# Optimization experiments

Measured on AMD Instinct MI355X. Metric: run time of the kernel, lower is better.

Reference implementation:

```python
import jax, jax.numpy as jnp
import numpy as np

B, H, L, D = 4, 16, 2048, 64


def setup_inputs() -> dict:
    key = jax.random.key(0)
    k1, k2, k3 = jax.random.split(key, 3)
    return {
        "query": jax.random.normal(k1, (B, H, L, D), dtype=jnp.float32),
        "key": jax.random.normal(k2, (B, H, L, D), dtype=jnp.float32),
        "value": jax.random.normal(k3, (B, H, D, L), dtype=jnp.float32),
    }


def reference(query, key, value):
    # dot_product_score = Q @ K^T / sqrt(D)   -> [B,H,L,L]
    d = query.shape[-1]
    scores = jnp.einsum("bhqd,bhkd->bhqk", query, key) / jnp.sqrt(jnp.asarray(d, query.dtype))
    attn = jax.nn.softmax(scores, axis=-1)
    # NOTE: original module returns matmul(value, attention_score) = V @ A
    # (value contracted over its last dim L with attn's query dim L) -> [B,H,D,L]
    return jnp.matmul(value, attn)
```

## Files before the change

### kernel.cpp

```cpp
#include <hip/hip_runtime.h>
#include <hip/hip_bf16.h>

#define L_SEQ 2048
#define D_HEAD 64
#define NHEADS 64
#define QSCALE (0.125f * 1.44269504088896340736f)

typedef __attribute__((ext_vector_type(8))) __bf16 bf16x8;
typedef __attribute__((ext_vector_type(16))) float f32x16;

__device__ __forceinline__ int swz(int row, int col) {
    int off = (row << 7) | (col << 1);
    return off ^ ((row & 7) << 4);
}
__device__ __forceinline__ bf16x8 read_frag(const char* lds, int row, int col) {
    return *reinterpret_cast<const bf16x8*>(lds + swz(row, col));
}

template <int ROWS>
__device__ __forceinline__ void stage_load(float4* regs, const float* src,
                                           int srcStride, int t) {
    int r0 = t >> 4, c4 = (t & 15) << 2;
#pragma unroll
    for (int i = 0; i < ROWS / 16; ++i)
        regs[i] = *reinterpret_cast<const float4*>(src + (size_t)(r0 + i * 16) * srcStride + c4);
}
template <int ROWS>
__device__ __forceinline__ void stage_write(char* lds, const float4* regs, int t,
                                            float scale) {
    int r0 = t >> 4, c4 = (t & 15) << 2;
#pragma unroll
    for (int i = 0; i < ROWS / 16; ++i) {
        float4 v = regs[i];
        union { __bf16 h[4]; unsigned long long u; } pk;
        pk.h[0] = (__bf16)(v.x * scale);
        pk.h[1] = (__bf16)(v.y * scale);
        pk.h[2] = (__bf16)(v.z * scale);
        pk.h[3] = (__bf16)(v.w * scale);
        *reinterpret_cast<unsigned long long*>(lds + swz(r0 + i * 16, c4)) = pk.u;
    }
}

__device__ __forceinline__ unsigned cvt_pk_bf16(float lo, float hi) {
    unsigned r;
    asm("v_cvt_pk_bf16_f32 %0, %1, %2" : "=v"(r) : "v"(lo), "v"(hi));
    return r;
}

__global__ __launch_bounds__(256, 3) void attn_pass1(const float* __restrict__ Q,
                                                     const float* __restrict__ K,
                                                     float* __restrict__ invl) {
    __shared__ __align__(16) char lds[2][128 * 128];
    __shared__ float red[4][64];

    int bid = blockIdx.x;
    int sb = (bid & 7) * 256 + (bid >> 3);
    int bh = sb >> 5;
    int q0 = (sb & 31) << 6;
    const float* Qh = Q + (size_t)bh * L_SEQ * D_HEAD + (size_t)q0 * D_HEAD;
    const float* Kh = K + (size_t)bh * L_SEQ * D_HEAD;

    int t = threadIdx.x, lane = t & 63, w = t >> 6;
    int hl = lane >> 5, l31 = lane & 31;

    {
        float4 qreg[4];
        stage_load<64>(qreg, Qh, D_HEAD, t);
        stage_write<64>(lds[0], qreg, t, QSCALE);
    }
    __syncthreads();
    bf16x8 qfrag[2][4];
#pragma unroll
    for (int qb = 0; qb < 2; ++qb)
#pragma unroll
        for (int m = 0; m < 4; ++m)
            qfrag[qb][m] = read_frag(lds[0], qb * 32 + l31, m * 16 + hl * 8);
    __syncthreads();
    {
        float4 kreg[8];
        stage_load<128>(kreg, Kh, D_HEAD, t);
        stage_write<128>(lds[0], kreg, t, 1.0f);
    }
    __syncthreads();

    float lsum[2][16];
#pragma unroll
    for (int qb = 0; qb < 2; ++qb)
#pragma unroll
        for (int r = 0; r < 16; ++r) lsum[qb][r] = 0.f;

    for (int k0 = 0; k0 < L_SEQ; k0 += 128) {
        int c = (k0 >> 7) & 1;
        const char* kcur = lds[c];
        char* knext = lds[c ^ 1];

        int nk0 = (k0 + 128) & (L_SEQ - 1);
        float4 kreg[8];
        stage_load<128>(kreg, Kh + (size_t)nk0 * D_HEAD, D_HEAD, t);

        bf16x8 kfr[4];
#pragma unroll
        for (int m = 0; m < 4; ++m)
            kfr[m] = read_frag(kcur, w * 32 + l31, m * 16 + hl * 8);

        f32x16 s[2];
#pragma unroll
        for (int qb = 0; qb < 2; ++qb)
#pragma unroll
            for (int r = 0; r < 16; ++r) s[qb][r] = 0.f;

        __builtin_amdgcn_s_setprio(1);
#pragma unroll
        for (int m = 0; m < 4; ++m) {
            s[0] = __builtin_amdgcn_mfma_f32_32x32x16_bf16(qfrag[0][m], kfr[m], s[0], 0, 0, 0);
            s[1] = __builtin_amdgcn_mfma_f32_32x32x16_bf16(qfrag[1][m], kfr[m], s[1], 0, 0, 0);
        }
        __builtin_amdgcn_s_setprio(0);

#pragma unroll
        for (int qb = 0; qb < 2; ++qb)
#pragma unroll
            for (int r = 0; r < 16; ++r)
                lsum[qb][r] += __builtin_amdgcn_exp2f(s[qb][r]);

        stage_write<128>(knext, kreg, t, 1.0f);
        __syncthreads();
    }

#pragma unroll
    for (int qb = 0; qb < 2; ++qb)
#pragma unroll
        for (int r = 0; r < 16; ++r) {
            float v = lsum[qb][r];
            v += __shfl_xor(v, 1);
            v += __shfl_xor(v, 2);
            v += __shfl_xor(v, 4);
            v += __shfl_xor(v, 8);
            v += __shfl_xor(v, 16);
            lsum[qb][r] = v;
        }
    if (l31 == 0) {
#pragma unroll
        for (int qb = 0; qb < 2; ++qb)
#pragma unroll
            for (int r = 0; r < 16; ++r)
                red[w][qb * 32 + (r & 3) + 8 * (r >> 2) + 4 * hl] = lsum[qb][r];
    }
    __syncthreads();
    if (t < 64) {
        float ssum = red[0][t] + red[1][t] + red[2][t] + red[3][t];
        invl[(size_t)bh * L_SEQ + q0 + t] = 1.0f / ssum;
    }
}

__global__ __launch_bounds__(256, 2) void attn_pass2(const float* __restrict__ Q,
                                                     const float* __restrict__ K,
                                                     const float* __restrict__ V,
                                                     const float* __restrict__ invl,
                                                     float* __restrict__ out) {
    __shared__ __align__(16) char lds[32768];
    char* ldsQ0 = lds;
    char* ldsQ1 = lds + 8192;
    char* ldsV0 = lds + 16384;
    char* ldsV1 = lds + 24576;

    int bid = blockIdx.x;
    int sb = (bid & 7) * 64 + (bid >> 3);
    int bh = sb >> 3;
    int k0 = (sb & 7) << 8;
    const float* Qh = Q + (size_t)bh * L_SEQ * D_HEAD;
    const float* Kh = K + (size_t)bh * L_SEQ * D_HEAD + (size_t)k0 * D_HEAD;
    const float* Vh = V + (size_t)bh * D_HEAD * L_SEQ;
    const float* il = invl + (size_t)bh * L_SEQ;
    float* Oh = out + (size_t)bh * D_HEAD * L_SEQ;

    int t = threadIdx.x, lane = t & 63, w = t >> 6;
    int hl = lane >> 5, l31 = lane & 31;

    {
        float4 kreg[8];
        stage_load<128>(kreg, Kh, D_HEAD, t);
        stage_write<128>(lds, kreg, t, 1.0f);
        stage_load<128>(kreg, Kh + (size_t)128 * D_HEAD, D_HEAD, t);
        stage_write<128>(lds + 128 * 128, kreg, t, 1.0f);
    }
    __syncthreads();
    bf16x8 kfrag[2][4];
#pragma unroll
    for (int kb = 0; kb < 2; ++kb)
#pragma unroll
        for (int m = 0; m < 4; ++m)
            kfrag[kb][m] = read_frag(lds, w * 64 + kb * 32 + l31, m * 16 + hl * 8);
    __syncthreads();
    {
        float4 qreg[4], vreg[4];
        stage_load<64>(qreg, Qh, D_HEAD, t);
        stage_load<64>(vreg, Vh, L_SEQ, t);
        stage_write<64>(ldsQ0, qreg, t, QSCALE);
        stage_write<64>(ldsV0, vreg, t, 1.0f);
    }
    __syncthreads();

    f32x16 acc[2][2];
#pragma unroll
    for (int db = 0; db < 2; ++db)
#pragma unroll
        for (int kb = 0; kb < 2; ++kb)
#pragma unroll
            for (int r = 0; r < 16; ++r) acc[db][kb][r] = 0.f;

    for (int q0 = 0; q0 < L_SEQ; q0 += 64) {
        int c = (q0 >> 6) & 1;
        const char* qcur = c ? ldsQ1 : ldsQ0;
        const char* vcur = c ? ldsV1 : ldsV0;
        char* qnext = c ? ldsQ0 : ldsQ1;
        char* vnext = c ? ldsV0 : ldsV1;

        int nq0 = (q0 + 64) & (L_SEQ - 1);
        float4 qreg[4], vreg[4];
        stage_load<64>(qreg, Qh + (size_t)nq0 * D_HEAD, D_HEAD, t);
        stage_load<64>(vreg, Vh + nq0, L_SEQ, t);

#pragma unroll
        for (int qb = 0; qb < 2; ++qb) {
            union { float4 v4[4]; float f[16]; } ilu;
#pragma unroll
            for (int g = 0; g < 4; ++g)
                ilu.v4[g] = *reinterpret_cast<const float4*>(il + q0 + qb * 32 + 8 * g + 4 * hl);

            f32x16 s[2];
#pragma unroll
            for (int kb = 0; kb < 2; ++kb)
#pragma unroll
                for (int r = 0; r < 16; ++r) s[kb][r] = 0.f;

            __builtin_amdgcn_s_setprio(1);
#pragma unroll
            for (int m = 0; m < 4; ++m) {
                bf16x8 afr = read_frag(qcur, qb * 32 + l31, m * 16 + hl * 8);
                s[0] = __builtin_amdgcn_mfma_f32_32x32x16_bf16(afr, kfrag[0][m], s[0], 0, 0, 0);
                s[1] = __builtin_amdgcn_mfma_f32_32x32x16_bf16(afr, kfrag[1][m], s[1], 0, 0, 0);
            }
            __builtin_amdgcn_s_setprio(0);

            bf16x8 pfrag[2][2];
#pragma unroll
            for (int kb = 0; kb < 2; ++kb) {
                float p[16];
#pragma unroll
                for (int r = 0; r < 16; ++r)
                    p[r] = __builtin_amdgcn_exp2f(s[kb][r]) * ilu.f[r];
                unsigned wA[4], wB[4];
#pragma unroll
                for (int g = 0; g < 4; ++g) {
                    wA[g] = cvt_pk_bf16(p[4 * g + 0], p[4 * g + 1]);
                    wB[g] = cvt_pk_bf16(p[4 * g + 2], p[4 * g + 3]);
                }
#pragma unroll
                for (int mm = 0; mm < 2; ++mm) {
                    unsigned a0 = wA[2 * mm], b0 = wA[2 * mm + 1];
                    unsigned a1 = wB[2 * mm], b1 = wB[2 * mm + 1];
                    asm volatile("v_permlane32_swap_b32 %0, %1" : "+v"(a0), "+v"(b0));
                    asm volatile("v_permlane32_swap_b32 %0, %1" : "+v"(a1), "+v"(b1));
                    union { unsigned u[4]; bf16x8 v; } pk;
                    pk.u[0] = a0;
                    pk.u[1] = a1;
                    pk.u[2] = b0;
                    pk.u[3] = b1;
                    pfrag[kb][mm] = pk.v;
                }
            }

            __builtin_amdgcn_s_setprio(1);
#pragma unroll
            for (int mm = 0; mm < 2; ++mm)
#pragma unroll
                for (int db = 0; db < 2; ++db) {
                    bf16x8 vfr = read_frag(vcur, db * 32 + l31, qb * 32 + mm * 16 + hl * 8);
#pragma unroll
                    for (int kb = 0; kb < 2; ++kb)
                        acc[db][kb] = __builtin_amdgcn_mfma_f32_32x32x16_bf16(
                            vfr, pfrag[kb][mm], acc[db][kb], 0, 0, 0);
                }
            __builtin_amdgcn_s_setprio(0);
        }

        stage_write<64>(qnext, qreg, t, QSCALE);
        stage_write<64>(vnext, vreg, t, 1.0f);
        __syncthreads();
    }

#pragma unroll
    for (int db = 0; db < 2; ++db)
#pragma unroll
        for (int kb = 0; kb < 2; ++kb)
#pragma unroll
            for (int r = 0; r < 16; ++r) {
                int d = db * 32 + (r & 3) + 8 * (r >> 2) + 4 * hl;
                int k = k0 + w * 64 + kb * 32 + l31;
                Oh[(size_t)d * L_SEQ + k] = acc[db][kb][r];
            }
}

extern "C" void kernel_launch(void* const* d_in, const int* in_sizes, int n_in,
                              void* d_out, int out_size, void* d_ws, size_t ws_size,
                              hipStream_t stream) {
    const float* Q = (const float*)d_in[0];
    const float* K = (const float*)d_in[1];
    const float* V = (const float*)d_in[2];
    float* invl = (float*)d_ws;
    float* out = (float*)d_out;

    attn_pass1<<<dim3(NHEADS * (L_SEQ / 64)), dim3(256), 0, stream>>>(Q, K, invl);
    attn_pass2<<<dim3(NHEADS * (L_SEQ / 256)), dim3(256), 0, stream>>>(Q, K, V, invl, out);
}
```

Measured before the change: 160.8 us.

## Split pass2 key tile over 8 waves and fold 1/l into V staging

Pass2 now launches 512 threads per block, so each of 8 waves owns 32 keys instead of 64. This halves per-wave accumulators and the K fragments held in registers, aiming for higher occupancy. The softmax normalizer 1/l is multiplied into V while it is converted to bf16 in LDS, which removes the per-element multiply after exp2. Each Q/V tile read from LDS is now shared by twice as many waves, which may add LDS traffic and barrier cost. Rounding V*invl to bf16 slightly changes precision.

```diff
diff --git a/kernel.cpp b/kernel.cpp
--- a/kernel.cpp
+++ b/kernel.cpp
@@ -41,6 +41,16 @@
     }
 }
 
+__device__ __forceinline__ void pack_write(char* lds, int row, int c4, float4 v,
+                                           float4 sc) {
+    union { __bf16 h[4]; unsigned long long u; } pk;
+    pk.h[0] = (__bf16)(v.x * sc.x);
+    pk.h[1] = (__bf16)(v.y * sc.y);
+    pk.h[2] = (__bf16)(v.z * sc.z);
+    pk.h[3] = (__bf16)(v.w * sc.w);
+    *reinterpret_cast<unsigned long long*>(lds + swz(row, c4)) = pk.u;
+}
+
 __device__ __forceinline__ unsigned cvt_pk_bf16(float lo, float hi) {
     unsigned r;
     asm("v_cvt_pk_bf16_f32 %0, %1, %2" : "=v"(r) : "v"(lo), "v"(hi));
@@ -153,16 +163,12 @@
     }
 }
 
-__global__ __launch_bounds__(256, 2) void attn_pass2(const float* __restrict__ Q,
+__global__ __launch_bounds__(512, 4) void attn_pass2(const float* __restrict__ Q,
                                                      const float* __restrict__ K,
                                                      const float* __restrict__ V,
                                                      const float* __restrict__ invl,
                                                      float* __restrict__ out) {
     __shared__ __align__(16) char lds[32768];
-    char* ldsQ0 = lds;
-    char* ldsQ1 = lds + 8192;
-    char* ldsV0 = lds + 16384;
-    char* ldsV1 = lds + 24576;
 
     int bid = blockIdx.x;
     int sb = (bid & 7) * 64 + (bid >> 3);
@@ -176,130 +182,123 @@
 
     int t = threadIdx.x, lane = t & 63, w = t >> 6;
     int hl = lane >> 5, l31 = lane & 31;
+    int r0 = t >> 4;
+    int c4 = (t & 15) << 2;
+
+#pragma unroll
+    for (int i = 0; i < 8; ++i) {
+        float4 v = *reinterpret_cast<const float4*>(Kh + (size_t)(r0 + i * 32) * D_HEAD + c4);
+        pack_write(lds, r0 + i * 32, c4, v, make_float4(1.f, 1.f, 1.f, 1.f));
+    }
+    __syncthreads();
+    bf16x8 kfrag[4];
+#pragma unroll
+    for (int m = 0; m < 4; ++m)
+        kfrag[m] = read_frag(lds, w * 32 + l31, m * 16 + hl * 8);
+    __syncthreads();
 
     {
-        float4 kreg[8];
-        stage_load<128>(kreg, Kh, D_HEAD, t);
-        stage_write<128>(lds, kreg, t, 1.0f);
-        stage_load<128>(kreg, Kh + (size_t)128 * D_HEAD, D_HEAD, t);
-        stage_write<128>(lds + 128 * 128, kreg, t, 1.0f);
-    }
-    __syncthreads();
-    bf16x8 kfrag[2][4];
-#pragma unroll
-    for (int kb = 0; kb < 2; ++kb)
-#pragma unroll
-        for (int m = 0; m < 4; ++m)
-            kfrag[kb][m] = read_frag(lds, w * 64 + kb * 32 + l31, m * 16 + hl * 8);
-    __syncthreads();
-    {
-        float4 qreg[4], vreg[4];
-        stage_load<64>(qreg, Qh, D_HEAD, t);
-        stage_load<64>(vreg, Vh, L_SEQ, t);
-        stage_write<64>(ldsQ0, qreg, t, QSCALE);
-        stage_write<64>(ldsV0, vreg, t, 1.0f);
-    }
-    __syncthreads();
-
-    f32x16 acc[2][2];
+        float4 qa = *reinterpret_cast<const float4*>(Qh + (size_t)r0 * D_HEAD + c4);
+        float4 qb = *reinterpret_cast<const float4*>(Qh + (size_t)(r0 + 32) * D_HEAD + c4);
+        float4 va = *reinterpret_cast<const float4*>(Vh + (size_t)r0 * L_SEQ + c4);
+        float4 vb = *reinterpret_cast<const float4*>(Vh + (size_t)(r0 + 32) * L_SEQ + c4);
+        float4 iv = *reinterpret_cast<const float4*>(il + c4);
+        float4 qs = make_float4(QSCALE, QSCALE, QSCALE, QSCALE);
+        pack_write(lds, r0, c4, qa, qs);
+        pack_write(lds, r0 + 32, c4, qb, qs);
+        pack_write(lds + 16384, r0, c4, va, iv);
+        pack_write(lds + 16384, r0 + 32, c4, vb, iv);
+    }
+    __syncthreads();
+
+    f32x16 acc[2];
 #pragma unroll
     for (int db = 0; db < 2; ++db)
 #pragma unroll
-        for (int kb = 0; kb < 2; ++kb)
-#pragma unroll
-            for (int r = 0; r < 16; ++r) acc[db][kb][r] = 0.f;
+        for (int r = 0; r < 16; ++r) acc[db][r] = 0.f;
 
     for (int q0 = 0; q0 < L_SEQ; q0 += 64) {
         int c = (q0 >> 6) & 1;
-        const char* qcur = c ? ldsQ1 : ldsQ0;
-        const char* vcur = c ? ldsV1 : ldsV0;
-        char* qnext = c ? ldsQ0 : ldsQ1;
-        char* vnext = c ? ldsV0 : ldsV1;
+        const char* qcur = c ? lds + 8192 : lds;
+        const char* vcur = c ? lds + 24576 : lds + 16384;
+        char* qnext = c ? lds : lds + 8192;
+        char* vnext = c ? lds + 16384 : lds + 24576;
 
         int nq0 = (q0 + 64) & (L_SEQ - 1);
-        float4 qreg[4], vreg[4];
-        stage_load<64>(qreg, Qh + (size_t)nq0 * D_HEAD, D_HEAD, t);
-        stage_load<64>(vreg, Vh + nq0, L_SEQ, t);
-
-#pragma unroll
-        for (int qb = 0; qb < 2; ++qb) {
-            union { float4 v4[4]; float f[16]; } ilu;
-#pragma unroll
-            for (int g = 0; g < 4; ++g)
-                ilu.v4[g] = *reinterpret_cast<const float4*>(il + q0 + qb * 32 + 8 * g + 4 * hl);
-
-            f32x16 s[2];
-#pragma unroll
-            for (int kb = 0; kb < 2; ++kb)
-#pragma unroll
-                for (int r = 0; r < 16; ++r) s[kb][r] = 0.f;
+        float4 qra = *reinterpret_cast<const float4*>(Qh + (size_t)(nq0 + r0) * D_HEAD + c4);
+        float4 qrb = *reinterpret_cast<const float4*>(Qh + (size_t)(nq0 + r0 + 32) * D_HEAD + c4);
+        float4 vra = *reinterpret_cast<const float4*>(Vh + (size_t)r0 * L_SEQ + nq0 + c4);
+        float4 vrb = *reinterpret_cast<const float4*>(Vh + (size_t)(r0 + 32) * L_SEQ + nq0 + c4);
+        float4 ivn = *reinterpret_cast<const float4*>(il + nq0 + c4);
+
+#pragma unroll
+        for (int qq = 0; qq < 2; ++qq) {
+            f32x16 s;
+#pragma unroll
+            for (int r = 0; r < 16; ++r) s[r] = 0.f;
 
             __builtin_amdgcn_s_setprio(1);
 #pragma unroll
             for (int m = 0; m < 4; ++m) {
-                bf16x8 afr = read_frag(qcur, qb * 32 + l31, m * 16 + hl * 8);
-                s[0] = __builtin_amdgcn_mfma_f32_32x32x16_bf16(afr, kfrag[0][m], s[0], 0, 0, 0);
-                s[1] = __builtin_amdgcn_mfma_f32_32x32x16_bf16(afr, kfrag[1][m], s[1], 0, 0, 0);
+                bf16x8 afr = read_frag(qcur, qq * 32 + l31, m * 16 + hl * 8);
+                s = __builtin_amdgcn_mfma_f32_32x32x16_bf16(afr, kfrag[m], s, 0, 0, 0);
             }
             __builtin_amdgcn_s_setprio(0);
 
-            bf16x8 pfrag[2][2];
-#pragma unroll
-            for (int kb = 0; kb < 2; ++kb) {
-                float p[16];
-#pragma unroll
-                for (int r = 0; r < 16; ++r)
-                    p[r] = __builtin_amdgcn_exp2f(s[kb][r]) * ilu.f[r];
-                unsigned wA[4], wB[4];
-#pragma unroll
-                for (int g = 0; g < 4; ++g) {
-                    wA[g] = cvt_pk_bf16(p[4 * g + 0], p[4 * g + 1]);
-                    wB[g] = cvt_pk_bf16(p[4 * g + 2], p[4 * g + 3]);
-                }
-#pragma unroll
-                for (int mm = 0; mm < 2; ++mm) {
-                    unsigned a0 = wA[2 * mm], b0 = wA[2 * mm + 1];
-                    unsigned a1 = wB[2 * mm], b1 = wB[2 * mm + 1];
-                    asm volatile("v_permlane32_swap_b32 %0, %1" : "+v"(a0), "+v"(b0));
-                    asm volatile("v_permlane32_swap_b32 %0, %1" : "+v"(a1), "+v"(b1));
-                    union { unsigned u[4]; bf16x8 v; } pk;
-                    pk.u[0] = a0;
-                    pk.u[1] = a1;
-                    pk.u[2] = b0;
-                    pk.u[3] = b1;
-                    pfrag[kb][mm] = pk.v;
-                }
+            float p[16];
+#pragma unroll
+            for (int r = 0; r < 16; ++r) p[r] = __builtin_amdgcn_exp2f(s[r]);
+            unsigned wA[4], wB[4];
+#pragma unroll
+            for (int g = 0; g < 4; ++g) {
+                wA[g] = cvt_pk_bf16(p[4 * g + 0], p[4 * g + 1]);
+                wB[g] = cvt_pk_bf16(p[4 * g + 2], p[4 * g + 3]);
             }
+            bf16x8 pfrag[2];
+#pragma unroll
+            for (int mm = 0; mm < 2; ++mm) {
+                unsigned a0 = wA[2 * mm], b0 = wA[2 * mm + 1];
+                unsigned a1 = wB[2 * mm], b1 = wB[2 * mm + 1];
+                asm volatile("v_permlane32_swap_b32 %0, %1" : "+v"(a0), "+v"(b0));
+                asm volatile("v_permlane32_swap_b32 %0, %1" : "+v"(a1), "+v"(b1));
+                union { unsigned u[4]; bf16x8 v; } pk;
+                pk.u[0] = a0;
+                pk.u[1] = a1;
+                pk.u[2] = b0;
+                pk.u[3] = b1;
+                pfrag[mm] = pk.v;
+            }
 
             __builtin_amdgcn_s_setprio(1);
 #pragma unroll
             for (int mm = 0; mm < 2; ++mm)
 #pragma unroll
                 for (int db = 0; db < 2; ++db) {
-                    bf16x8 vfr = read_frag(vcur, db * 32 + l31, qb * 32 + mm * 16 + hl * 8);
-#pragma unroll
-                    for (int kb = 0; kb < 2; ++kb)
-                        acc[db][kb] = __builtin_amdgcn_mfma_f32_32x32x16_bf16(
-                            vfr, pfrag[kb][mm], acc[db][kb], 0, 0, 0);
+                    bf16x8 vfr = read_frag(vcur, db * 32 + l31, qq * 32 + mm * 16 + hl * 8);
+                    acc[db] = __builtin_amdgcn_mfma_f32_32x32x16_bf16(
+                        vfr, pfrag[mm], acc[db], 0, 0, 0);
                 }
             __builtin_amdgcn_s_setprio(0);
         }
 
-        stage_write<64>(qnext, qreg, t, QSCALE);
-        stage_write<64>(vnext, vreg, t, 1.0f);
+        {
+            float4 qs = make_float4(QSCALE, QSCALE, QSCALE, QSCALE);
+            pack_write(qnext, r0, c4, qra, qs);
+            pack_write(qnext, r0 + 32, c4, qrb, qs);
+            pack_write(vnext, r0, c4, vra, ivn);
+            pack_write(vnext, r0 + 32, c4, vrb, ivn);
+        }
         __syncthreads();
     }
 
 #pragma unroll
     for (int db = 0; db < 2; ++db)
 #pragma unroll
-        for (int kb = 0; kb < 2; ++kb)
-#pragma unroll
-            for (int r = 0; r < 16; ++r) {
-                int d = db * 32 + (r & 3) + 8 * (r >> 2) + 4 * hl;
-                int k = k0 + w * 64 + kb * 32 + l31;
-                Oh[(size_t)d * L_SEQ + k] = acc[db][kb][r];
-            }
+        for (int r = 0; r < 16; ++r) {
+            int d = db * 32 + (r & 3) + 8 * (r >> 2) + 4 * hl;
+            int k = k0 + w * 32 + l31;
+            Oh[(size_t)d * L_SEQ + k] = acc[db][r];
+        }
 }
 
 extern "C" void kernel_launch(void* const* d_in, const int* in_sizes, int n_in,
@@ -312,5 +311,5 @@
     float* out = (float*)d_out;
 
     attn_pass1<<<dim3(NHEADS * (L_SEQ / 64)), dim3(256), 0, stream>>>(Q, K, invl);
-    attn_pass2<<<dim3(NHEADS * (L_SEQ / 256)), dim3(256), 0, stream>>>(Q, K, V, invl, out);
-}
+    attn_pass2<<<dim3(NHEADS * (L_SEQ / 256)), dim3(512), 0, stream>>>(Q, K, V, invl, out);
+}
```

New measurement: 158.5 us. Within noise of the previous version (-1.4%).

## Split pass2 over 128-key tiles with query-split waves and fold 1/l into V

Applied to the files above, without the earlier changes.

Pass2 now gives each block 128 keys instead of 256, which doubles the grid. Each pair of waves shares a key slice while splitting the 64-query chunk in two, and the halves' partial outputs are reduced through LDS at the end. The softmax normalizer 1/l is now folded into V when it is converted to bf16 in LDS, so it is no longer multiplied into every probability in the inner loop. Occupancy is raised to 3 blocks per CU. In exchange, Q/V staging traffic per output doubles and the kernel adds an LDS reduction epilogue.

```diff
diff --git a/kernel.cpp b/kernel.cpp
--- a/kernel.cpp
+++ b/kernel.cpp
@@ -41,6 +41,16 @@
     }
 }
 
+__device__ __forceinline__ void pack_write(char* lds, int row, int c4, float4 v,
+                                           float4 sc) {
+    union { __bf16 h[4]; unsigned long long u; } pk;
+    pk.h[0] = (__bf16)(v.x * sc.x);
+    pk.h[1] = (__bf16)(v.y * sc.y);
+    pk.h[2] = (__bf16)(v.z * sc.z);
+    pk.h[3] = (__bf16)(v.w * sc.w);
+    *reinterpret_cast<unsigned long long*>(lds + swz(row, c4)) = pk.u;
+}
+
 __device__ __forceinline__ unsigned cvt_pk_bf16(float lo, float hi) {
     unsigned r;
     asm("v_cvt_pk_bf16_f32 %0, %1, %2" : "=v"(r) : "v"(lo), "v"(hi));
@@ -91,8 +101,8 @@
 
     for (int k0 = 0; k0 < L_SEQ; k0 += 128) {
         int c = (k0 >> 7) & 1;
-        const char* kcur = lds[c];
-        char* knext = lds[c ^ 1];
+        const char* kcur = c ? lds[1] : lds[0];
+        char* knext = c ? lds[0] : lds[1];
 
         int nk0 = (k0 + 128) & (L_SEQ - 1);
         float4 kreg[8];
@@ -153,21 +163,17 @@
     }
 }
 
-__global__ __launch_bounds__(256, 2) void attn_pass2(const float* __restrict__ Q,
+__global__ __launch_bounds__(256, 3) void attn_pass2(const float* __restrict__ Q,
                                                      const float* __restrict__ K,
                                                      const float* __restrict__ V,
                                                      const float* __restrict__ invl,
                                                      float* __restrict__ out) {
-    __shared__ __align__(16) char lds[32768];
-    char* ldsQ0 = lds;
-    char* ldsQ1 = lds + 8192;
-    char* ldsV0 = lds + 16384;
-    char* ldsV1 = lds + 24576;
+    __shared__ __align__(16) char lds[49152];
 
     int bid = blockIdx.x;
-    int sb = (bid & 7) * 64 + (bid >> 3);
-    int bh = sb >> 3;
-    int k0 = (sb & 7) << 8;
+    int sb = (bid & 7) * 128 + (bid >> 3);
+    int bh = sb >> 4;
+    int k0 = (sb & 15) << 7;
     const float* Qh = Q + (size_t)bh * L_SEQ * D_HEAD;
     const float* Kh = K + (size_t)bh * L_SEQ * D_HEAD + (size_t)k0 * D_HEAD;
     const float* Vh = V + (size_t)bh * D_HEAD * L_SEQ;
@@ -175,14 +181,15 @@
     float* Oh = out + (size_t)bh * D_HEAD * L_SEQ;
 
     int t = threadIdx.x, lane = t & 63, w = t >> 6;
+    int wq = w >> 1, wk = w & 1;
     int hl = lane >> 5, l31 = lane & 31;
+    int r0 = t >> 4;
+    int c4 = (t & 15) << 2;
 
     {
         float4 kreg[8];
         stage_load<128>(kreg, Kh, D_HEAD, t);
         stage_write<128>(lds, kreg, t, 1.0f);
-        stage_load<128>(kreg, Kh + (size_t)128 * D_HEAD, D_HEAD, t);
-        stage_write<128>(lds + 128 * 128, kreg, t, 1.0f);
     }
     __syncthreads();
     bf16x8 kfrag[2][4];
@@ -190,14 +197,19 @@
     for (int kb = 0; kb < 2; ++kb)
 #pragma unroll
         for (int m = 0; m < 4; ++m)
-            kfrag[kb][m] = read_frag(lds, w * 64 + kb * 32 + l31, m * 16 + hl * 8);
-    __syncthreads();
+            kfrag[kb][m] = read_frag(lds, wk * 64 + kb * 32 + l31, m * 16 + hl * 8);
+
     {
         float4 qreg[4], vreg[4];
         stage_load<64>(qreg, Qh, D_HEAD, t);
         stage_load<64>(vreg, Vh, L_SEQ, t);
-        stage_write<64>(ldsQ0, qreg, t, QSCALE);
-        stage_write<64>(ldsV0, vreg, t, 1.0f);
+        float4 iv = *reinterpret_cast<const float4*>(il + c4);
+        float4 qs = make_float4(QSCALE, QSCALE, QSCALE, QSCALE);
+#pragma unroll
+        for (int i = 0; i < 4; ++i) {
+            pack_write(lds + 16384, r0 + i * 16, c4, qreg[i], qs);
+            pack_write(lds + 24576, r0 + i * 16, c4, vreg[i], iv);
+        }
     }
     __syncthreads();
 
@@ -211,95 +223,109 @@
 
     for (int q0 = 0; q0 < L_SEQ; q0 += 64) {
         int c = (q0 >> 6) & 1;
-        const char* qcur = c ? ldsQ1 : ldsQ0;
-        const char* vcur = c ? ldsV1 : ldsV0;
-        char* qnext = c ? ldsQ0 : ldsQ1;
-        char* vnext = c ? ldsV0 : ldsV1;
+        const char* qcur = lds + (c ? 32768 : 16384);
+        const char* vcur = lds + (c ? 40960 : 24576);
+        char* qnext = lds + (c ? 16384 : 32768);
+        char* vnext = lds + (c ? 24576 : 40960);
 
         int nq0 = (q0 + 64) & (L_SEQ - 1);
         float4 qreg[4], vreg[4];
         stage_load<64>(qreg, Qh + (size_t)nq0 * D_HEAD, D_HEAD, t);
         stage_load<64>(vreg, Vh + nq0, L_SEQ, t);
 
-#pragma unroll
-        for (int qb = 0; qb < 2; ++qb) {
-            union { float4 v4[4]; float f[16]; } ilu;
-#pragma unroll
-            for (int g = 0; g < 4; ++g)
-                ilu.v4[g] = *reinterpret_cast<const float4*>(il + q0 + qb * 32 + 8 * g + 4 * hl);
-
-            f32x16 s[2];
+        f32x16 s[2];
+#pragma unroll
+        for (int kb = 0; kb < 2; ++kb)
+#pragma unroll
+            for (int r = 0; r < 16; ++r) s[kb][r] = 0.f;
+
+        __builtin_amdgcn_s_setprio(1);
+#pragma unroll
+        for (int m = 0; m < 4; ++m) {
+            bf16x8 afr = read_frag(qcur, wq * 32 + l31, m * 16 + hl * 8);
+            s[0] = __builtin_amdgcn_mfma_f32_32x32x16_bf16(afr, kfrag[0][m], s[0], 0, 0, 0);
+            s[1] = __builtin_amdgcn_mfma_f32_32x32x16_bf16(afr, kfrag[1][m], s[1], 0, 0, 0);
+        }
+        __builtin_amdgcn_s_setprio(0);
+
+        bf16x8 pfrag[2][2];
+#pragma unroll
+        for (int kb = 0; kb < 2; ++kb) {
+            float p[16];
+#pragma unroll
+            for (int r = 0; r < 16; ++r) p[r] = __builtin_amdgcn_exp2f(s[kb][r]);
+            unsigned wA[4], wB[4];
+#pragma unroll
+            for (int g = 0; g < 4; ++g) {
+                wA[g] = cvt_pk_bf16(p[4 * g + 0], p[4 * g + 1]);
+                wB[g] = cvt_pk_bf16(p[4 * g + 2], p[4 * g + 3]);
+            }
+#pragma unroll
+            for (int mm = 0; mm < 2; ++mm) {
+                unsigned a0 = wA[2 * mm], b0 = wA[2 * mm + 1];
+                unsigned a1 = wB[2 * mm], b1 = wB[2 * mm + 1];
+                asm volatile("v_permlane32_swap_b32 %0, %1" : "+v"(a0), "+v"(b0));
+                asm volatile("v_permlane32_swap_b32 %0, %1" : "+v"(a1), "+v"(b1));
+                union { unsigned u[4]; bf16x8 v; } pk;
+                pk.u[0] = a0;
+                pk.u[1] = a1;
+                pk.u[2] = b0;
+                pk.u[3] = b1;
+                pfrag[kb][mm] = pk.v;
+            }
+        }
+
+        __builtin_amdgcn_s_setprio(1);
+#pragma unroll
+        for (int mm = 0; mm < 2; ++mm)
+#pragma unroll
+            for (int db = 0; db < 2; ++db) {
+                bf16x8 vfr = read_frag(vcur, db * 32 + l31, wq * 32 + mm * 16 + hl * 8);
+#pragma unroll
+                for (int kb = 0; kb < 2; ++kb)
+                    acc[db][kb] = __builtin_amdgcn_mfma_f32_32x32x16_bf16(
+                        vfr, pfrag[kb][mm], acc[db][kb], 0, 0, 0);
+            }
+        __builtin_amdgcn_s_setprio(0);
+
+        {
+            float4 ivn = *reinterpret_cast<const float4*>(il + nq0 + c4);
+            float4 qs = make_float4(QSCALE, QSCALE, QSCALE, QSCALE);
+#pragma unroll
+            for (int i = 0; i < 4; ++i) {
+                pack_write(qnext, r0 + i * 16, c4, qreg[i], qs);
+                pack_write(vnext, r0 + i * 16, c4, vreg[i], ivn);
+            }
+        }
+        __syncthreads();
+    }
+
+    __syncthreads();
+    float* exf = reinterpret_cast<float*>(lds + 16384);
+    if (wq == 1) {
+#pragma unroll
+        for (int db = 0; db < 2; ++db)
 #pragma unroll
             for (int kb = 0; kb < 2; ++kb)
 #pragma unroll
-                for (int r = 0; r < 16; ++r) s[kb][r] = 0.f;
-
-            __builtin_amdgcn_s_setprio(1);
-#pragma unroll
-            for (int m = 0; m < 4; ++m) {
-                bf16x8 afr = read_frag(qcur, qb * 32 + l31, m * 16 + hl * 8);
-                s[0] = __builtin_amdgcn_mfma_f32_32x32x16_bf16(afr, kfrag[0][m], s[0], 0, 0, 0);
-                s[1] = __builtin_amdgcn_mfma_f32_32x32x16_bf16(afr, kfrag[1][m], s[1], 0, 0, 0);
-            }
-            __builtin_amdgcn_s_setprio(0);
-
-            bf16x8 pfrag[2][2];
-#pragma unroll
-            for (int kb = 0; kb < 2; ++kb) {
-                float p[16];
-#pragma unroll
                 for (int r = 0; r < 16; ++r)
-                    p[r] = __builtin_amdgcn_exp2f(s[kb][r]) * ilu.f[r];
-                unsigned wA[4], wB[4];
-#pragma unroll
-                for (int g = 0; g < 4; ++g) {
-                    wA[g] = cvt_pk_bf16(p[4 * g + 0], p[4 * g + 1]);
-                    wB[g] = cvt_pk_bf16(p[4 * g + 2], p[4 * g + 3]);
+                    exf[(((wk * 2 + db) * 2 + kb) * 16 + r) * 64 + lane] = acc[db][kb][r];
+    }
+    __syncthreads();
+    if (wq == 0) {
+#pragma unroll
+        for (int db = 0; db < 2; ++db)
+#pragma unroll
+            for (int kb = 0; kb < 2; ++kb)
+#pragma unroll
+                for (int r = 0; r < 16; ++r) {
+                    float v = acc[db][kb][r] +
+                              exf[(((wk * 2 + db) * 2 + kb) * 16 + r) * 64 + lane];
+                    int d = db * 32 + (r & 3) + 8 * (r >> 2) + 4 * hl;
+                    int k = k0 + wk * 64 + kb * 32 + l31;
+                    Oh[(size_t)d * L_SEQ + k] = v;
                 }
-#pragma unroll
-                for (int mm = 0; mm < 2; ++mm) {
-                    unsigned a0 = wA[2 * mm], b0 = wA[2 * mm + 1];
-                    unsigned a1 = wB[2 * mm], b1 = wB[2 * mm + 1];
-                    asm volatile("v_permlane32_swap_b32 %0, %1" : "+v"(a0), "+v"(b0));
-                    asm volatile("v_permlane32_swap_b32 %0, %1" : "+v"(a1), "+v"(b1));
-                    union { unsigned u[4]; bf16x8 v; } pk;
-                    pk.u[0] = a0;
-                    pk.u[1] = a1;
-                    pk.u[2] = b0;
-                    pk.u[3] = b1;
-                    pfrag[kb][mm] = pk.v;
-                }
-            }
-
-            __builtin_amdgcn_s_setprio(1);
-#pragma unroll
-            for (int mm = 0; mm < 2; ++mm)
-#pragma unroll
-                for (int db = 0; db < 2; ++db) {
-                    bf16x8 vfr = read_frag(vcur, db * 32 + l31, qb * 32 + mm * 16 + hl * 8);
-#pragma unroll
-                    for (int kb = 0; kb < 2; ++kb)
-                        acc[db][kb] = __builtin_amdgcn_mfma_f32_32x32x16_bf16(
-                            vfr, pfrag[kb][mm], acc[db][kb], 0, 0, 0);
-                }
-            __builtin_amdgcn_s_setprio(0);
-        }
-
-        stage_write<64>(qnext, qreg, t, QSCALE);
-        stage_write<64>(vnext, vreg, t, 1.0f);
-        __syncthreads();
-    }
-
-#pragma unroll
-    for (int db = 0; db < 2; ++db)
-#pragma unroll
-        for (int kb = 0; kb < 2; ++kb)
-#pragma unroll
-            for (int r = 0; r < 16; ++r) {
-                int d = db * 32 + (r & 3) + 8 * (r >> 2) + 4 * hl;
-                int k = k0 + w * 64 + kb * 32 + l31;
-                Oh[(size_t)d * L_SEQ + k] = acc[db][kb][r];
-            }
+    }
 }
 
 extern "C" void kernel_launch(void* const* d_in, const int* in_sizes, int n_in,
@@ -312,5 +338,5 @@
     float* out = (float*)d_out;
 
     attn_pass1<<<dim3(NHEADS * (L_SEQ / 64)), dim3(256), 0, stream>>>(Q, K, invl);
-    attn_pass2<<<dim3(NHEADS * (L_SEQ / 256)), dim3(256), 0, stream>>>(Q, K, V, invl, out);
-}
+    attn_pass2<<<dim3(NHEADS * (L_SEQ / 128)), dim3(256), 0, stream>>>(Q, K, V, invl, out);
+}
```

Result: slower. 291.8 us (+81.5%).
